# Optimization experiments

Hardware: AMD Instinct MI355X
Metric: run time of the kernel (lower is better)

The kernel has to match this reference:

```python
import jax, jax.numpy as jnp
import numpy as np

N_NODES = 50000
N_EDGES = 1600000
D = 128
LEAKY_SLOPE = 0.01  # torch nn.LeakyReLU default


def setup_inputs() -> dict:
    key = jax.random.key(0)
    ks = jax.random.split(key, 7)
    entity_embed = jax.random.normal(ks[0], (N_NODES, D), dtype=jnp.float32)
    W1 = jax.random.normal(ks[1], (D, D), dtype=jnp.float32) * 0.05
    b1 = jax.random.normal(ks[2], (D,), dtype=jnp.float32) * 0.05
    W2 = jax.random.normal(ks[3], (D, D), dtype=jnp.float32) * 0.05
    b2 = jax.random.normal(ks[4], (D,), dtype=jnp.float32) * 0.05
    src = jax.random.randint(ks[5], (N_EDGES,), 0, N_NODES, dtype=jnp.int32)
    dst = jax.random.randint(ks[6], (N_EDGES,), 0, N_NODES, dtype=jnp.int32)
    return {"entity_embed": entity_embed, "W1": W1, "b1": b1,
            "W2": W2, "b2": b2, "src": src, "dst": dst}


def reference(entity_embed, W1, b1, W2, b2, src, dst):
    # DGL update_all(copy_u('node','side'), sum('side','H')):
    # H[v] = sum over edges (u -> v) of entity_embed[u]
    n = entity_embed.shape[0]
    H = jax.ops.segment_sum(entity_embed[src], dst, num_segments=n)  # [N, D]
    # neighbors branch: LeakyReLU(W_1 @ H)
    neighbors = jax.nn.leaky_relu(H @ W1.T + b1, negative_slope=LEAKY_SLOPE)
    # interactions branch: LeakyReLU(W_2 @ (node * H))
    interactions = jax.nn.leaky_relu((entity_embed * H) @ W2.T + b2,
                                     negative_slope=LEAKY_SLOPE)
    # dropout is identity at inference
    return neighbors + interactions
```

## Files before the change

### kernel.cpp

```cpp
#include <hip/hip_runtime.h>

#define NN 50000
#define DD 128
#define SLOPE 0.01f
#define NB 782
#define BCAP 2560
#define ECH 8192
#define OVCAP 8192

using bf16x8 = __attribute__((ext_vector_type(8))) short;
using f32x4  = __attribute__((ext_vector_type(4))) float;

__device__ inline float bflo(unsigned int w) { return __uint_as_float(w << 16); }
__device__ inline float bfhi(unsigned int w) { return __uint_as_float(w & 0xffff0000u); }
__device__ inline unsigned int rnebf(float f) {
    unsigned int u = __float_as_uint(f);
    return (u + 0x7fffu + ((u >> 16) & 1u)) >> 16;
}
__device__ inline unsigned int pack2(float lo, float hi) {
    return rnebf(lo) | (rnebf(hi) << 16);
}
__device__ inline void unpack8(uint4 r, float* f) {
    f[0] = bflo(r.x); f[1] = bfhi(r.x); f[2] = bflo(r.y); f[3] = bfhi(r.y);
    f[4] = bflo(r.z); f[5] = bfhi(r.z); f[6] = bflo(r.w); f[7] = bfhi(r.w);
}
__device__ inline uint4 pack8(const float* f) {
    uint4 o;
    o.x = pack2(f[0], f[1]); o.y = pack2(f[2], f[3]);
    o.z = pack2(f[4], f[5]); o.w = pack2(f[6], f[7]);
    return o;
}
__device__ inline void addrow(float* acc, uint4 r) {
    acc[0] += bflo(r.x); acc[1] += bfhi(r.x);
    acc[2] += bflo(r.y); acc[3] += bfhi(r.y);
    acc[4] += bflo(r.z); acc[5] += bfhi(r.z);
    acc[6] += bflo(r.w); acc[7] += bfhi(r.w);
}

__global__ __launch_bounds__(256) void convert_bf(
    const float* __restrict__ E, const float* __restrict__ W1,
    const float* __restrict__ W2, unsigned short* __restrict__ Ebf,
    unsigned short* __restrict__ W1b, unsigned short* __restrict__ W2b)
{
    const int NE8 = NN * DD / 8;
    const int NW8 = DD * DD / 8;
    int t = blockIdx.x * 256 + threadIdx.x;
    const float* s; unsigned short* d; int idx;
    if (t < NE8)                { s = E;  d = Ebf; idx = t; }
    else if (t < NE8 + NW8)     { s = W1; d = W1b; idx = t - NE8; }
    else if (t < NE8 + 2 * NW8) { s = W2; d = W2b; idx = t - NE8 - NW8; }
    else return;
    float4 a = ((const float4*)s)[(size_t)idx * 2];
    float4 b = ((const float4*)s)[(size_t)idx * 2 + 1];
    uint4 o;
    o.x = pack2(a.x, a.y); o.y = pack2(a.z, a.w);
    o.z = pack2(b.x, b.y); o.w = pack2(b.z, b.w);
    ((uint4*)d)[idx] = o;
}

__global__ __launch_bounds__(256) void bin_sort(
    const int* __restrict__ src, const int* __restrict__ dst,
    int* __restrict__ gtail, unsigned int* __restrict__ stag,
    int* __restrict__ ovf_cnt, int2* __restrict__ ovf, int n_edges)
{
    __shared__ unsigned int srt[ECH];
    __shared__ int cnt[NB], off[NB], pos[NB];
    __shared__ int wsum[4];

    const int tid = threadIdx.x;
    const int e0 = blockIdx.x * ECH;
    const int m = min(ECH, n_edges - e0);

    for (int b = tid; b < NB; b += 256) cnt[b] = 0;
    __syncthreads();

    for (int i = tid; i < m; i += 256)
        atomicAdd(&cnt[dst[e0 + i] >> 6], 1);
    __syncthreads();

    const int lane = tid & 63, w = tid >> 6;
    int b0 = tid * 4;
    int loc[4]; int s = 0;
    #pragma unroll
    for (int j = 0; j < 4; ++j) {
        int bb = b0 + j;
        int cv = (bb < NB) ? cnt[bb] : 0;
        loc[j] = s; s += cv;
    }
    int incl = s;
    #pragma unroll
    for (int d = 1; d < 64; d <<= 1) {
        int t2 = __shfl_up(incl, d);
        if (lane >= d) incl += t2;
    }
    if (lane == 63) wsum[w] = incl;
    __syncthreads();
    int wbase = 0;
    for (int w2 = 0; w2 < w; ++w2) wbase += wsum[w2];
    int base = wbase + incl - s;
    #pragma unroll
    for (int j = 0; j < 4; ++j) {
        int bb = b0 + j;
        if (bb < NB) { off[bb] = base + loc[j]; pos[bb] = base + loc[j]; }
    }
    __syncthreads();

    for (int i = tid; i < m; i += 256) {
        int v = dst[e0 + i];
        int u = src[e0 + i];
        int p = atomicAdd(&pos[v >> 6], 1);
        srt[p] = (unsigned int)u | ((unsigned int)(v & 63) << 16);
    }
    __syncthreads();

    for (int bb = tid; bb < NB; bb += 256) {
        int c = cnt[bb];
        if (!c) continue;
        int g = atomicAdd(&gtail[bb], c);
        int s0 = off[bb];
        unsigned int* dstp = stag + (size_t)bb * BCAP;
        for (int k = 0; k < c; ++k) {
            int gp = g + k;
            unsigned int r = srt[s0 + k];
            if (gp < BCAP) {
                dstp[gp] = r;
            } else {
                int oi = atomicAdd(ovf_cnt, 1);
                if (oi < OVCAP)
                    ovf[oi] = make_int2((int)(r & 0xffffu),
                                        bb * 64 + (int)((r >> 16) & 63));
            }
        }
    }
}

__global__ __launch_bounds__(256) void bucket_gather(
    const unsigned short* __restrict__ Ebf, const int* __restrict__ gtail,
    const unsigned int* __restrict__ stag, unsigned short* __restrict__ Hb,
    unsigned short* __restrict__ EHb)
{
    __shared__ unsigned short sorted[BCAP];
    __shared__ int cnt[64], off[65], pos[64];

    const int b = blockIdx.x;
    const int tid = threadIdx.x;
    int len = gtail[b]; len = len < BCAP ? len : BCAP;
    const unsigned int* seg = stag + (size_t)b * BCAP;

    if (tid < 64) cnt[tid] = 0;
    __syncthreads();
    for (int i = tid; i < len; i += 256)
        atomicAdd(&cnt[(seg[i] >> 16) & 63], 1);
    __syncthreads();
    if (tid == 0) {
        int a = 0;
        for (int j = 0; j < 64; ++j) { off[j] = a; pos[j] = a; a += cnt[j]; }
        off[64] = a;
    }
    __syncthreads();
    for (int i = tid; i < len; i += 256) {
        unsigned int r = seg[i];
        int p = atomicAdd(&pos[(r >> 16) & 63], 1);
        sorted[p] = (unsigned short)(r & 0xffffu);
    }
    __syncthreads();

    const int g = tid >> 4;
    const int c = tid & 15;
    const uint4* E4 = (const uint4*)Ebf;
    for (int p4 = 0; p4 < 4; ++p4) {
        int nl = p4 * 16 + g;
        int v = b * 64 + nl;
        if (v >= NN) continue;
        float acc[8] = {};
        int i = off[nl], e1 = off[nl + 1];
        for (; i + 4 <= e1; i += 4) {
            uint4 r0 = E4[(size_t)sorted[i]     * 16 + c];
            uint4 r1 = E4[(size_t)sorted[i + 1] * 16 + c];
            uint4 r2 = E4[(size_t)sorted[i + 2] * 16 + c];
            uint4 r3 = E4[(size_t)sorted[i + 3] * 16 + c];
            addrow(acc, r0); addrow(acc, r1); addrow(acc, r2); addrow(acc, r3);
        }
        for (; i < e1; ++i) addrow(acc, E4[(size_t)sorted[i] * 16 + c]);

        float ef[8]; unpack8(E4[(size_t)v * 16 + c], ef);
        float eh[8];
        #pragma unroll
        for (int j = 0; j < 8; ++j) eh[j] = ef[j] * acc[j];
        ((uint4*)Hb)[(size_t)v * 16 + c] = pack8(acc);
        ((uint4*)EHb)[(size_t)v * 16 + c] = pack8(eh);
    }
}

__global__ void fix_overflow_bf(
    const int* __restrict__ ovf_cnt, const int2* __restrict__ ovf,
    const unsigned short* __restrict__ Ebf, unsigned short* __restrict__ Hb,
    unsigned short* __restrict__ EHb)
{
    int total = *ovf_cnt; total = total < OVCAP ? total : OVCAP;
    if (total == 0) return;
    int c = threadIdx.x;
    if (c >= 16) return;
    for (int i = 0; i < total; ++i) {
        int u = ovf[i].x, v = ovf[i].y;
        float hf[8], ef[8], evf[8], eh[8];
        unpack8(((const uint4*)Hb)[(size_t)v * 16 + c], hf);
        unpack8(((const uint4*)Ebf)[(size_t)u * 16 + c], ef);
        #pragma unroll
        for (int j = 0; j < 8; ++j) hf[j] += ef[j];
        ((uint4*)Hb)[(size_t)v * 16 + c] = pack8(hf);
        unpack8(((const uint4*)Ebf)[(size_t)v * 16 + c], evf);
        #pragma unroll
        for (int j = 0; j < 8; ++j) eh[j] = evf[j] * hf[j];
        ((uint4*)EHb)[(size_t)v * 16 + c] = pack8(eh);
    }
}

__global__ __launch_bounds__(256) void gemm_bf(
    const unsigned short* __restrict__ Hb, const unsigned short* __restrict__ EHb,
    const unsigned short* __restrict__ W1b, const unsigned short* __restrict__ W2b,
    const float* __restrict__ b1, const float* __restrict__ b2,
    float* __restrict__ out)
{
    const int wave = threadIdx.x >> 6;
    const int lane = threadIdx.x & 63;
    const int v0 = blockIdx.x * 64 + wave * 16;
    if (v0 >= NN) return;
    const int m = lane & 15;
    const int quad = lane >> 4;

    bf16x8 aH[4], aE[4];
    const unsigned short* hrow = Hb  + (size_t)(v0 + m) * DD + quad * 8;
    const unsigned short* erow = EHb + (size_t)(v0 + m) * DD + quad * 8;
    #pragma unroll
    for (int ks = 0; ks < 4; ++ks) {
        aH[ks] = *(const bf16x8*)(hrow + ks * 32);
        aE[ks] = *(const bf16x8*)(erow + ks * 32);
    }

    #pragma unroll
    for (int jt = 0; jt < 8; ++jt) {
        const int j0 = jt * 16;
        const unsigned short* w1r = W1b + (size_t)(j0 + m) * DD + quad * 8;
        const unsigned short* w2r = W2b + (size_t)(j0 + m) * DD + quad * 8;
        f32x4 acc1 = {0.f, 0.f, 0.f, 0.f}, acc2 = {0.f, 0.f, 0.f, 0.f};
        #pragma unroll
        for (int ks = 0; ks < 4; ++ks) {
            bf16x8 bw1 = *(const bf16x8*)(w1r + ks * 32);
            bf16x8 bw2 = *(const bf16x8*)(w2r + ks * 32);
            acc1 = __builtin_amdgcn_mfma_f32_16x16x32_bf16(aH[ks], bw1, acc1, 0, 0, 0);
            acc2 = __builtin_amdgcn_mfma_f32_16x16x32_bf16(aE[ks], bw2, acc2, 0, 0, 0);
        }
        const float bb1 = b1[j0 + m], bb2 = b2[j0 + m];
        #pragma unroll
        for (int i = 0; i < 4; ++i) {
            float x1 = acc1[i] + bb1; x1 = x1 > 0.f ? x1 : SLOPE * x1;
            float x2 = acc2[i] + bb2; x2 = x2 > 0.f ? x2 : SLOPE * x2;
            out[(size_t)(v0 + quad * 4 + i) * DD + j0 + m] = x1 + x2;
        }
    }
}

__global__ __launch_bounds__(256) void scatter_add(
    const float* __restrict__ E, const int* __restrict__ src,
    const int* __restrict__ dst, float* __restrict__ H, int n_edges)
{
    int t = blockIdx.x * 256 + threadIdx.x;
    int e = t >> 5;
    if (e >= n_edges) return;
    int c = t & 31;
    float4 a = ((const float4*)E)[(size_t)src[e] * 32 + c];
    float* hp = H + (size_t)dst[e] * DD + c * 4;
    atomicAdd(hp + 0, a.x); atomicAdd(hp + 1, a.y);
    atomicAdd(hp + 2, a.z); atomicAdd(hp + 3, a.w);
}

__global__ __launch_bounds__(256) void fused_mlp(
    const float* __restrict__ E, const float* __restrict__ H,
    const float* __restrict__ W1, const float* __restrict__ b1,
    const float* __restrict__ W2, const float* __restrict__ b2,
    float* __restrict__ out)
{
    __shared__ float Hs[32][DD];
    __shared__ float EHs[32][DD];
    __shared__ float W1s[DD][20];
    __shared__ float W2s[DD][20];
    const int tid = threadIdx.x;
    const int v0 = blockIdx.x * 32;
    const int nvalid = min(32, NN - v0);
    for (int i = 0; i < 4; ++i) {
        int f = tid + 256 * i;
        int n = f >> 5, c = f & 31;
        float4 h = make_float4(0.f, 0.f, 0.f, 0.f);
        float4 eh = h;
        if (n < nvalid) {
            h = ((const float4*)H)[(size_t)(v0 + n) * 32 + c];
            float4 e4 = ((const float4*)E)[(size_t)(v0 + n) * 32 + c];
            eh = make_float4(e4.x * h.x, e4.y * h.y, e4.z * h.z, e4.w * h.w);
        }
        *((float4*)&Hs[n][c * 4]) = h;
        *((float4*)&EHs[n][c * 4]) = eh;
    }
    const int jg = tid & 63;
    const int n0 = (tid >> 6) * 8;
    float acc1a[8] = {}, acc1b[8] = {}, acc2a[8] = {}, acc2b[8] = {};
    for (int t8 = 0; t8 < 8; ++t8) {
        const int k0 = t8 * 16;
        __syncthreads();
        for (int i = 0; i < 8; ++i) {
            int f = tid + 256 * i;
            int j = f >> 4, kk = f & 15;
            W1s[j][kk] = W1[j * DD + k0 + kk];
            W2s[j][kk] = W2[j * DD + k0 + kk];
        }
        __syncthreads();
        for (int c = 0; c < 4; ++c) {
            float4 w1a = *((const float4*)&W1s[jg][c * 4]);
            float4 w1b = *((const float4*)&W1s[jg + 64][c * 4]);
            float4 w2a = *((const float4*)&W2s[jg][c * 4]);
            float4 w2b = *((const float4*)&W2s[jg + 64][c * 4]);
            const int kk = k0 + c * 4;
            for (int n = 0; n < 8; ++n) {
                float4 h = *((const float4*)&Hs[n0 + n][kk]);
                float4 eh = *((const float4*)&EHs[n0 + n][kk]);
                acc1a[n] += h.x * w1a.x + h.y * w1a.y + h.z * w1a.z + h.w * w1a.w;
                acc1b[n] += h.x * w1b.x + h.y * w1b.y + h.z * w1b.z + h.w * w1b.w;
                acc2a[n] += eh.x * w2a.x + eh.y * w2a.y + eh.z * w2a.z + eh.w * w2a.w;
                acc2b[n] += eh.x * w2b.x + eh.y * w2b.y + eh.z * w2b.z + eh.w * w2b.w;
            }
        }
    }
    const float b1a = b1[jg], b1b = b1[jg + 64];
    const float b2a = b2[jg], b2b = b2[jg + 64];
    for (int n = 0; n < 8; ++n) {
        if (n0 + n < nvalid) {
            const int v = v0 + n0 + n;
            float x1 = acc1a[n] + b1a; x1 = x1 > 0.f ? x1 : SLOPE * x1;
            float x2 = acc2a[n] + b2a; x2 = x2 > 0.f ? x2 : SLOPE * x2;
            out[(size_t)v * DD + jg] = x1 + x2;
            float y1 = acc1b[n] + b1b; y1 = y1 > 0.f ? y1 : SLOPE * y1;
            float y2 = acc2b[n] + b2b; y2 = y2 > 0.f ? y2 : SLOPE * y2;
            out[(size_t)v * DD + jg + 64] = y1 + y2;
        }
    }
}

extern "C" void kernel_launch(void* const* d_in, const int* in_sizes, int n_in,
                              void* d_out, int out_size, void* d_ws, size_t ws_size,
                              hipStream_t stream)
{
    const float* E  = (const float*)d_in[0];
    const float* W1 = (const float*)d_in[1];
    const float* b1 = (const float*)d_in[2];
    const float* W2 = (const float*)d_in[3];
    const float* b2 = (const float*)d_in[4];
    const int* src  = (const int*)d_in[5];
    const int* dst  = (const int*)d_in[6];
    float* out = (float*)d_out;
    const int n_edges = in_sizes[5];

    char* ws = (char*)d_ws;
    auto al = [](size_t x) { return (x + 255) & ~(size_t)255; };

    const size_t off_tail = 0;
    const size_t off_ovfc = (size_t)NB * 4;
    const size_t off_ovf  = al(off_ovfc + 4);
    const size_t off_stag = al(off_ovf + (size_t)OVCAP * 8);
    const size_t off_Ebf  = al(off_stag + (size_t)NB * BCAP * 4);
    const size_t off_Hb   = al(off_Ebf + (size_t)NN * DD * 2);
    const size_t off_EHb  = al(off_Hb + (size_t)NN * DD * 2);
    const size_t off_W1b  = al(off_EHb + (size_t)NN * DD * 2);
    const size_t off_W2b  = al(off_W1b + (size_t)DD * DD * 2);
    const size_t need_bf  = off_W2b + (size_t)DD * DD * 2;

    if (ws_size >= need_bf) {
        int*  gtail   = (int*)(ws + off_tail);
        int*  ovf_cnt = (int*)(ws + off_ovfc);
        int2* ovf     = (int2*)(ws + off_ovf);
        unsigned int*   stag = (unsigned int*)(ws + off_stag);
        unsigned short* Ebf  = (unsigned short*)(ws + off_Ebf);
        unsigned short* Hb   = (unsigned short*)(ws + off_Hb);
        unsigned short* EHb  = (unsigned short*)(ws + off_EHb);
        unsigned short* W1b  = (unsigned short*)(ws + off_W1b);
        unsigned short* W2b  = (unsigned short*)(ws + off_W2b);

        hipMemsetAsync(ws, 0, off_ovf, stream);
        const int ncv = NN * DD / 8 + 2 * (DD * DD / 8);
        convert_bf<<<(ncv + 255) / 256, 256, 0, stream>>>(E, W1, W2, Ebf, W1b, W2b);
        bin_sort<<<(n_edges + ECH - 1) / ECH, 256, 0, stream>>>(
            src, dst, gtail, stag, ovf_cnt, ovf, n_edges);
        bucket_gather<<<NB, 256, 0, stream>>>(Ebf, gtail, stag, Hb, EHb);
        fix_overflow_bf<<<1, 64, 0, stream>>>(ovf_cnt, ovf, Ebf, Hb, EHb);
        gemm_bf<<<(NN + 63) / 64, 256, 0, stream>>>(Hb, EHb, W1b, W2b, b1, b2, out);
        return;
    }

    const size_t hbytes = (size_t)NN * DD * sizeof(float);
    float* H = (ws_size >= hbytes) ? (float*)ws : out;
    hipMemsetAsync(H, 0, hbytes, stream);
    scatter_add<<<((n_edges * 32) + 255) / 256, 256, 0, stream>>>(
        E, src, dst, H, n_edges);
    fused_mlp<<<(NN + 31) / 32, 256, 0, stream>>>(E, H, W1, b1, W2, b2, out);
}
```

Measured before the change: 218.5 us.

## Split bucket gather into half-buckets and widen bin sort blocks

Bucket_gather now launches two blocks per 64-node bucket, each re-scanning the full bucket staging list but keeping only edges for its 32 nodes, which doubles the block count for better occupancy and latency hiding. The gather loop is unrolled to 8 outstanding row loads with a 2-wide tail. Bin_sort uses 512-thread blocks with smaller 6144-edge chunks, giving more blocks and more threads per chunk. The cost is that every bucket's staging data is read twice, and smaller chunks mean more global atomics on bucket tails.

```diff
diff --git a/kernel.cpp b/kernel.cpp
--- a/kernel.cpp
+++ b/kernel.cpp
@@ -5,7 +5,9 @@
 #define SLOPE 0.01f
 #define NB 782
 #define BCAP 2560
-#define ECH 8192
+#define ECH 6144
+#define BST 512
+#define PB 2
 #define OVCAP 8192
 
 using bf16x8 = __attribute__((ext_vector_type(8))) short;
@@ -58,31 +60,31 @@
     ((uint4*)d)[idx] = o;
 }
 
-__global__ __launch_bounds__(256) void bin_sort(
+__global__ __launch_bounds__(BST) void bin_sort(
     const int* __restrict__ src, const int* __restrict__ dst,
     int* __restrict__ gtail, unsigned int* __restrict__ stag,
     int* __restrict__ ovf_cnt, int2* __restrict__ ovf, int n_edges)
 {
     __shared__ unsigned int srt[ECH];
     __shared__ int cnt[NB], off[NB], pos[NB];
-    __shared__ int wsum[4];
+    __shared__ int wsum[BST / 64];
 
     const int tid = threadIdx.x;
     const int e0 = blockIdx.x * ECH;
     const int m = min(ECH, n_edges - e0);
 
-    for (int b = tid; b < NB; b += 256) cnt[b] = 0;
-    __syncthreads();
-
-    for (int i = tid; i < m; i += 256)
+    for (int b = tid; b < NB; b += BST) cnt[b] = 0;
+    __syncthreads();
+
+    for (int i = tid; i < m; i += BST)
         atomicAdd(&cnt[dst[e0 + i] >> 6], 1);
     __syncthreads();
 
     const int lane = tid & 63, w = tid >> 6;
-    int b0 = tid * 4;
-    int loc[4]; int s = 0;
+    int b0 = tid * PB;
+    int loc[PB]; int s = 0;
     #pragma unroll
-    for (int j = 0; j < 4; ++j) {
+    for (int j = 0; j < PB; ++j) {
         int bb = b0 + j;
         int cv = (bb < NB) ? cnt[bb] : 0;
         loc[j] = s; s += cv;
@@ -99,13 +101,13 @@
     for (int w2 = 0; w2 < w; ++w2) wbase += wsum[w2];
     int base = wbase + incl - s;
     #pragma unroll
-    for (int j = 0; j < 4; ++j) {
+    for (int j = 0; j < PB; ++j) {
         int bb = b0 + j;
         if (bb < NB) { off[bb] = base + loc[j]; pos[bb] = base + loc[j]; }
     }
     __syncthreads();
 
-    for (int i = tid; i < m; i += 256) {
+    for (int i = tid; i < m; i += BST) {
         int v = dst[e0 + i];
         int u = src[e0 + i];
         int p = atomicAdd(&pos[v >> 6], 1);
@@ -113,7 +115,7 @@
     }
     __syncthreads();
 
-    for (int bb = tid; bb < NB; bb += 256) {
+    for (int bb = tid; bb < NB; bb += BST) {
         int c = cnt[bb];
         if (!c) continue;
         int g = atomicAdd(&gtail[bb], c);
@@ -140,48 +142,64 @@
     unsigned short* __restrict__ EHb)
 {
     __shared__ unsigned short sorted[BCAP];
-    __shared__ int cnt[64], off[65], pos[64];
-
-    const int b = blockIdx.x;
+    __shared__ int cnt[32], off[33], pos[32];
+
+    const int b = blockIdx.x >> 1;
+    const int half = blockIdx.x & 1;
     const int tid = threadIdx.x;
     int len = gtail[b]; len = len < BCAP ? len : BCAP;
     const unsigned int* seg = stag + (size_t)b * BCAP;
 
-    if (tid < 64) cnt[tid] = 0;
-    __syncthreads();
-    for (int i = tid; i < len; i += 256)
-        atomicAdd(&cnt[(seg[i] >> 16) & 63], 1);
+    if (tid < 32) cnt[tid] = 0;
+    __syncthreads();
+    for (int i = tid; i < len; i += 256) {
+        int nl = (seg[i] >> 16) & 63;
+        if ((nl >> 5) == half) atomicAdd(&cnt[nl & 31], 1);
+    }
     __syncthreads();
     if (tid == 0) {
         int a = 0;
-        for (int j = 0; j < 64; ++j) { off[j] = a; pos[j] = a; a += cnt[j]; }
-        off[64] = a;
+        for (int j = 0; j < 32; ++j) { off[j] = a; pos[j] = a; a += cnt[j]; }
+        off[32] = a;
     }
     __syncthreads();
     for (int i = tid; i < len; i += 256) {
         unsigned int r = seg[i];
-        int p = atomicAdd(&pos[(r >> 16) & 63], 1);
-        sorted[p] = (unsigned short)(r & 0xffffu);
+        int nl = (r >> 16) & 63;
+        if ((nl >> 5) == half) {
+            int p = atomicAdd(&pos[nl & 31], 1);
+            sorted[p] = (unsigned short)(r & 0xffffu);
+        }
     }
     __syncthreads();
 
     const int g = tid >> 4;
     const int c = tid & 15;
     const uint4* E4 = (const uint4*)Ebf;
-    for (int p4 = 0; p4 < 4; ++p4) {
-        int nl = p4 * 16 + g;
-        int v = b * 64 + nl;
+    for (int p2 = 0; p2 < 2; ++p2) {
+        int nl = p2 * 16 + g;
+        int v = b * 64 + half * 32 + nl;
         if (v >= NN) continue;
         float acc[8] = {};
         int i = off[nl], e1 = off[nl + 1];
-        for (; i + 4 <= e1; i += 4) {
+        for (; i + 8 <= e1; i += 8) {
             uint4 r0 = E4[(size_t)sorted[i]     * 16 + c];
             uint4 r1 = E4[(size_t)sorted[i + 1] * 16 + c];
             uint4 r2 = E4[(size_t)sorted[i + 2] * 16 + c];
             uint4 r3 = E4[(size_t)sorted[i + 3] * 16 + c];
+            uint4 r4 = E4[(size_t)sorted[i + 4] * 16 + c];
+            uint4 r5 = E4[(size_t)sorted[i + 5] * 16 + c];
+            uint4 r6 = E4[(size_t)sorted[i + 6] * 16 + c];
+            uint4 r7 = E4[(size_t)sorted[i + 7] * 16 + c];
             addrow(acc, r0); addrow(acc, r1); addrow(acc, r2); addrow(acc, r3);
-        }
-        for (; i < e1; ++i) addrow(acc, E4[(size_t)sorted[i] * 16 + c]);
+            addrow(acc, r4); addrow(acc, r5); addrow(acc, r6); addrow(acc, r7);
+        }
+        for (; i + 2 <= e1; i += 2) {
+            uint4 r0 = E4[(size_t)sorted[i]     * 16 + c];
+            uint4 r1 = E4[(size_t)sorted[i + 1] * 16 + c];
+            addrow(acc, r0); addrow(acc, r1);
+        }
+        if (i < e1) addrow(acc, E4[(size_t)sorted[i] * 16 + c]);
 
         float ef[8]; unpack8(E4[(size_t)v * 16 + c], ef);
         float eh[8];
@@ -387,9 +405,9 @@
         hipMemsetAsync(ws, 0, off_ovf, stream);
         const int ncv = NN * DD / 8 + 2 * (DD * DD / 8);
         convert_bf<<<(ncv + 255) / 256, 256, 0, stream>>>(E, W1, W2, Ebf, W1b, W2b);
-        bin_sort<<<(n_edges + ECH - 1) / ECH, 256, 0, stream>>>(
+        bin_sort<<<(n_edges + ECH - 1) / ECH, BST, 0, stream>>>(
             src, dst, gtail, stag, ovf_cnt, ovf, n_edges);
-        bucket_gather<<<NB, 256, 0, stream>>>(Ebf, gtail, stag, Hb, EHb);
+        bucket_gather<<<NB * 2, 256, 0, stream>>>(Ebf, gtail, stag, Hb, EHb);
         fix_overflow_bf<<<1, 64, 0, stream>>>(ovf_cnt, ovf, Ebf, Hb, EHb);
         gemm_bf<<<(NN + 63) / 64, 256, 0, stream>>>(Hb, EHb, W1b, W2b, b1, b2, out);
         return;
```

After: 215.0 us. Within noise of the previous version (-1.6%).
